# Performance work log

Measured on AMD Instinct MI355X. Metric: run time of the kernel, lower is better.

The kernel has to match this reference:

```python
import jax, jax.numpy as jnp
import numpy as np

DIM = 768
NUM_HEADS = 12
HEAD_DIM = DIM // NUM_HEADS
WS = 14                       # window_size (14, 14)
N_TOK = WS * WS + 1           # 197 (patches + cls)
NUM_REL = (2 * WS - 1) ** 2 + 3  # 732
SCALE = HEAD_DIM ** -0.5


def _build_rel_index():
    # Faithful port of the BEiT relative_position_index construction.
    coords = np.stack(np.meshgrid(np.arange(WS), np.arange(WS), indexing='ij'))  # (2, WS, WS)
    flat = coords.reshape(2, -1)                                   # (2, WS*WS)
    rel = flat[:, :, None] - flat[:, None, :]                      # (2, P, P)
    rel = rel.transpose(1, 2, 0).astype(np.int64)                  # (P, P, 2)
    rel[:, :, 0] += WS - 1
    rel[:, :, 1] += WS - 1
    rel[:, :, 0] *= 2 * WS - 1
    idx = np.zeros((N_TOK, N_TOK), dtype=np.int64)
    idx[1:, 1:] = rel.sum(-1)
    idx[0, :] = NUM_REL - 3
    idx[:, 0] = NUM_REL - 2
    idx[0, 0] = NUM_REL - 1
    return idx


def setup_inputs() -> dict:
    key = jax.random.key(0)
    ks = jax.random.split(key, 7)
    B = 64
    x = jax.random.normal(ks[0], (B, N_TOK, DIM), dtype=jnp.float32)
    qkv_w = jax.random.normal(ks[1], (3 * DIM, DIM), dtype=jnp.float32) * 0.02
    q_bias = jnp.zeros((DIM,), dtype=jnp.float32)
    v_bias = jnp.zeros((DIM,), dtype=jnp.float32)
    rel_table = jax.random.normal(ks[2], (NUM_REL, NUM_HEADS), dtype=jnp.float32) * 0.02
    proj_w = jax.random.normal(ks[3], (DIM, DIM), dtype=jnp.float32) * 0.02
    proj_b = jnp.zeros((DIM,), dtype=jnp.float32)
    rel_index = jnp.asarray(_build_rel_index())  # (N, N) int64
    return {"x": x, "qkv_w": qkv_w, "q_bias": q_bias, "v_bias": v_bias,
            "rel_table": rel_table, "proj_w": proj_w, "proj_b": proj_b,
            "rel_index": rel_index}


def reference(x, qkv_w, q_bias, v_bias, rel_table, proj_w, proj_b, rel_index):
    B, N, C = x.shape
    # qkv bias = concat(q_bias, zeros, v_bias)
    qkv_b = jnp.concatenate([q_bias, jnp.zeros_like(v_bias), v_bias])
    qkv = x @ qkv_w.T + qkv_b                       # (B, N, 3C)
    qkv = qkv.reshape(B, N, 3, NUM_HEADS, HEAD_DIM).transpose(2, 0, 3, 1, 4)
    q, k, v = qkv[0], qkv[1], qkv[2]                # each (B, H, N, hd)
    attn = jnp.einsum('bhqd,bhkd->bhqk', q * SCALE, k)
    # relative position bias gathered from table: (N, N, H) -> (H, N, N)
    bias = rel_table[rel_index].transpose(2, 0, 1)
    attn = attn + bias[None]
    attn = jax.nn.softmax(attn, axis=-1)
    out = jnp.einsum('bhqk,bhkd->bhqd', attn, v)    # (B, H, N, hd)
    out = out.transpose(0, 2, 1, 3).reshape(B, N, -1)
    return out @ proj_w.T + proj_b
```

## Files before the change

### kernel.cpp

```cpp
#include <hip/hip_runtime.h>
#include <stdint.h>

#define NTOK 197
#define HD 64
#define NH 12
#define CDIM 768
#define BB 64
#define MTOT (BB*NTOK)
#define MPAD 12672
#define SCALE 0.125f
#define BTP 208

typedef __attribute__((ext_vector_type(8))) short short8;
typedef __attribute__((ext_vector_type(4))) float f32x4;
typedef unsigned short us;

__device__ __forceinline__ us f2b(float f){
    union { float f; uint32_t u; } v; v.f = f;
    uint32_t u = v.u;
    uint32_t r = u + 0x7fffu + ((u >> 16) & 1u);
    return (us)(r >> 16);
}

__device__ __forceinline__ float b2f(us b){
    union { uint32_t u; float f; } v; v.u = ((uint32_t)b) << 16;
    return v.f;
}

__device__ __forceinline__ void gload16(const us* g, us* l){
    __builtin_amdgcn_global_load_lds((const __attribute__((address_space(1))) void*)g,
                                     (__attribute__((address_space(3))) void*)l, 16, 0, 0);
}

#define LGKM0_BAR() do{ asm volatile("s_waitcnt lgkmcnt(0)" ::: "memory"); \
                        __builtin_amdgcn_s_barrier(); }while(0)

__device__ __forceinline__ void cvt4(const float* in, us* out, int i){
    float4 v = ((const float4*)in)[i];
    ushort4 o;
    o.x = f2b(v.x); o.y = f2b(v.y); o.z = f2b(v.z); o.w = f2b(v.w);
    ((ushort4*)out)[i] = o;
}

__global__ void prep_kernel(const float* __restrict__ x, const float* __restrict__ qkv_w,
                            const float* __restrict__ proj_w,
                            const int* __restrict__ rel_index, const float* __restrict__ rel_table,
                            us* __restrict__ xb, us* __restrict__ wqkv, us* __restrict__ wproj,
                            float* __restrict__ biasT)
{
    const int N1 = MTOT*CDIM/4;
    const int N2 = 3*CDIM*CDIM/4;
    const int N3 = CDIM*CDIM/4;
    const int N4 = BTP*BTP;
    const int total = N1+N2+N3+N4;
    for (int i = blockIdx.x*blockDim.x + threadIdx.x; i < total; i += gridDim.x*blockDim.x){
        if (i < N1) cvt4(x, xb, i);
        else if (i < N1+N2) cvt4(qkv_w, wqkv, i-N1);
        else if (i < N1+N2+N3) cvt4(proj_w, wproj, i-N1-N2);
        else {
            int t = i - N1 - N2 - N3;
            int col = t / BTP, row = t - col*BTP;
            if (row < NTOK && col < NTOK){
                int idx = rel_index[row*NTOK + col];
                #pragma unroll
                for (int h = 0; h < NH; ++h)
                    biasT[((size_t)h*BTP + col)*BTP + row] = rel_table[idx*NH + h];
            } else {
                #pragma unroll
                for (int h = 0; h < NH; ++h)
                    biasT[((size_t)h*BTP + col)*BTP + row] = 0.f;
            }
        }
    }
}

__global__ __launch_bounds__(512,2) void pgemm6_kernel(
    const us* __restrict__ A, const us* __restrict__ Bw,
    us* __restrict__ Qo, us* __restrict__ Ko, us* __restrict__ Vo,
    const float* __restrict__ b0, const float* __restrict__ b2, int ny, int total)
{
    __shared__ __align__(16) us AsB[3][12288];
    us* cbuf = &AsB[2][0];
    const int tid  = threadIdx.x;
    const int lane = tid & 63;
    const int wave = tid >> 6;
    const int wrr = wave >> 2;
    const int wcc = wave & 3;
    const int lr = lane & 15;
    const int g  = lane >> 4;

    const int id  = blockIdx.x;
    const int xcd = id & 7;
    const int jb  = id >> 3;
    const int qs  = total >> 3, rs = total & 7;
    const int Ssp = xcd*qs + (xcd < rs ? xcd : rs);
    const int L   = qs + (xcd < rs ? 1 : 0);
    const int qb  = L >> 6, rb = L & 63;
    const int cnt = qb + (jb < rb ? 1 : 0);
    const int w0  = Ssp + jb*qb + (jb < rb ? jb : rb);
    if (cnt == 0) return;

    int aoff, aldo, bofs[2], bldo[2];
    {
        int c = tid;
        int row = c >> 2, ch = c & 3;
        aoff = row*CDIM + ((ch ^ ((row >> 1) & 3))*8);
        aldo = c*8;
    }
    #pragma unroll
    for (int jj=0;jj<2;jj++){
        int c = tid + jj*512;
        int row = c >> 2, ch = c & 3;
        bofs[jj] = row*CDIM + ((ch ^ ((row >> 1) & 3))*8);
        bldo[jj] = 4096 + c*8;
    }

    const int S = cnt * 24;
    auto stageStep = [&](int x){
        int tt = x / 24, kt = x - tt*24;
        int ww = w0 + tt;
        int bx = ww / ny, by = ww - bx*ny;
        const us* pA = A  + (size_t)(bx*128)*CDIM;
        const us* pB = Bw + (size_t)(by*256)*CDIM;
        int buf = x % 3;
        gload16(pA + aoff + kt*32, &AsB[buf][aldo]);
        #pragma unroll
        for (int jj=0;jj<2;jj++) gload16(pB + bofs[jj] + kt*32, &AsB[buf][bldo[jj]]);
    };

    stageStep(0);
    if (S > 1) stageStep(1);
    int s = 0;

    const int co = 8*(g ^ ((lr >> 1) & 3));

    #pragma unroll 1
    for (int tt = 0; tt < cnt; ++tt){
        const int w  = w0 + tt;
        const int bx = w / ny, by = w - bx*ny;
        const int m0 = bx*128, n0 = by*256;
        const int whc = n0 / CDIM;
        float addf[4];
        const float sclf = (whc == 0) ? SCALE : 1.f;
        #pragma unroll
        for (int nt=0;nt<4;nt++){
            int n = n0 + wcc*64 + nt*16 + lr;
            int hn = n - whc*CDIM;
            addf[nt] = (whc == 0) ? b0[hn] : (whc == 2 ? b2[hn] : 0.f);
        }

        f32x4 acc[4][4];
        #pragma unroll
        for (int i=0;i<4;i++)
            #pragma unroll
            for (int jj=0;jj<4;jj++) acc[i][jj] = (f32x4){0.f,0.f,0.f,0.f};

        #pragma unroll 1
        for (int kt = 0; kt < 24; ++kt){
            if (s == S-1) asm volatile("s_waitcnt vmcnt(0)" ::: "memory");
            else          asm volatile("s_waitcnt vmcnt(3)" ::: "memory");
            __builtin_amdgcn_s_barrier();
            if (s + 2 < S) stageStep(s + 2);
            const us* la = &AsB[s % 3][0];
            const us* lb = &AsB[s % 3][4096];
            short8 af[4], bf[4];
            #pragma unroll
            for (int mt=0;mt<4;mt++)
                af[mt] = *(const short8*)&la[(wrr*64+mt*16+lr)*32 + co];
            #pragma unroll
            for (int nt=0;nt<4;nt++)
                bf[nt] = *(const short8*)&lb[(wcc*64+nt*16+lr)*32 + co];
            __builtin_amdgcn_s_setprio(1);
            #pragma unroll
            for (int mt=0;mt<4;mt++)
                #pragma unroll
                for (int nt=0;nt<4;nt++)
                    acc[mt][nt] = __builtin_amdgcn_mfma_f32_16x16x32_bf16(af[mt], bf[nt], acc[mt][nt], 0,0,0);
            __builtin_amdgcn_s_setprio(0);
            ++s;
        }

        LGKM0_BAR();

        const us* outp = (whc == 0 ? Qo : (whc == 1 ? Ko : Vo));
        #pragma unroll 1
        for (int ph = 0; ph < 4; ++ph){
            const int half  = ph & 1;
            const int rhalf = ph >> 1;
            if (wrr == rhalf && (wcc >> 1) == half){
                #pragma unroll
                for (int mt=0;mt<4;mt++)
                    #pragma unroll
                    for (int rr=0;rr<4;rr++){
                        int row = mt*16 + g*4 + rr;
                        #pragma unroll
                        for (int nt=0;nt<4;nt++){
                            int col = (wcc & 1)*64 + nt*16 + lr;
                            cbuf[row*132 + col] = f2b((acc[mt][nt][rr] + addf[nt]) * sclf);
                        }
                    }
            }
            LGKM0_BAR();
            #pragma unroll
            for (int p=0;p<2;p++){
                int c = tid + p*512;
                int row = c >> 4, ch = c & 15;
                int m = m0 + rhalf*64 + row;
                if (m < MTOT){
                    short8 vv = *(const short8*)&cbuf[row*132 + ch*8];
                    int n = n0 + half*128 + ch*8;
                    int hn = n - whc*CDIM;
                    int h  = hn >> 6, d0 = hn & 63;
                    int bidx = m / NTOK;
                    int tok  = m - bidx*NTOK;
                    size_t off = ((size_t)((bidx*NH + h)*NTOK + tok))*HD + d0;
                    *(short8*)((us*)outp + off) = vv;
                }
            }
            LGKM0_BAR();
        }
    }
}

__global__ __launch_bounds__(256) void proj_gemm_kernel(
    const us* __restrict__ A, const us* __restrict__ Bw,
    float* __restrict__ Cout, const float* __restrict__ b0, int ny)
{
    __shared__ __align__(16) us lds[32768];
    us* As = lds;
    us* Bs = lds + 16384;
    const int tid  = threadIdx.x;
    const int lane = tid & 63;
    const int wave = tid >> 6;
    const int wr = wave >> 1, wc = wave & 1;
    const int lr = lane & 15;
    const int g  = lane >> 4;

    const int NB   = gridDim.x;
    const int base = NB >> 3;
    const int rem  = NB & 7;
    const int id   = blockIdx.x;
    const int xcd  = id & 7;
    const int qq   = id >> 3;
    const int start = (xcd < rem) ? xcd*(base+1) : rem*(base+1) + (xcd-rem)*base;
    const int w    = start + qq;
    const int bx   = w / ny;
    const int by   = w - bx*ny;
    const int m0 = bx * 128;
    const int n0 = by * 128;
    const int NT = CDIM / 128;

    const int row0 = tid >> 4;
    const int cg   = (tid & 15) ^ row0;

    float addf[4];
    #pragma unroll
    for (int nt=0;nt<4;nt++) addf[nt] = b0[n0 + wc*64 + nt*16 + lr];

    f32x4 acc[4][4];
    #pragma unroll
    for (int i=0;i<4;i++)
        #pragma unroll
        for (int j=0;j<4;j++) acc[i][j] = (f32x4){0.f,0.f,0.f,0.f};

    const us* gA = A  + (size_t)(m0 + row0)*CDIM + cg*8;
    const us* gB = Bw + (size_t)(n0 + row0)*CDIM + cg*8;

    #pragma unroll 1
    for (int kt = 0; kt < NT; ++kt){
        __syncthreads();
        #pragma unroll
        for (int j=0;j<8;j++){
            gload16(gA + (size_t)j*16*CDIM + kt*128, As + tid*8 + j*2048);
            gload16(gB + (size_t)j*16*CDIM + kt*128, Bs + tid*8 + j*2048);
        }
        __syncthreads();
        #pragma unroll
        for (int kk=0; kk<4; ++kk){
            const int co = 8*((kk*4 + g) ^ lr);
            short8 af[4], bf[4];
            #pragma unroll
            for (int mt=0;mt<4;mt++)
                af[mt] = *(const short8*)&As[(wr*64+mt*16+lr)*128 + co];
            #pragma unroll
            for (int nt=0;nt<4;nt++)
                bf[nt] = *(const short8*)&Bs[(wc*64+nt*16+lr)*128 + co];
            __builtin_amdgcn_s_setprio(1);
            #pragma unroll
            for (int mt=0;mt<4;mt++)
                #pragma unroll
                for (int nt=0;nt<4;nt++)
                    acc[mt][nt] = __builtin_amdgcn_mfma_f32_16x16x32_bf16(af[mt], bf[nt], acc[mt][nt], 0,0,0);
            __builtin_amdgcn_s_setprio(0);
        }
    }

    __syncthreads();
    #pragma unroll
    for (int mt=0;mt<4;mt++)
        #pragma unroll
        for (int r=0;r<4;r++){
            int row = wr*64 + mt*16 + g*4 + r;
            #pragma unroll
            for (int nt=0;nt<4;nt++){
                int col = wc*64 + nt*16 + lr;
                lds[row*132 + col] = f2b(acc[mt][nt][r] + addf[nt]);
            }
        }
    __syncthreads();
    #pragma unroll
    for (int j=0;j<8;j++){
        int c2  = tid + j*256;
        int row = c2 >> 4;
        int ch  = c2 & 15;
        int m = m0 + row;
        if (m >= MTOT) continue;
        short8 vv = *(const short8*)&lds[row*132 + ch*8];
        int n = n0 + ch*8;
        float4 f0, f1;
        f0.x = b2f((us)vv[0]); f0.y = b2f((us)vv[1]); f0.z = b2f((us)vv[2]); f0.w = b2f((us)vv[3]);
        f1.x = b2f((us)vv[4]); f1.y = b2f((us)vv[5]); f1.z = b2f((us)vv[6]); f1.w = b2f((us)vv[7]);
        *(float4*)&Cout[(size_t)m*CDIM + n]     = f0;
        *(float4*)&Cout[(size_t)m*CDIM + n + 4] = f1;
    }
}

__global__ __launch_bounds__(256) void attn_kernel(
    const us* __restrict__ Q,
    const us* __restrict__ K,
    const us* __restrict__ V,
    const float* __restrict__ biasT,
    us* __restrict__ Ao)
{
    __shared__ us Vt[64][232];
    __shared__ us Ps[4][16][232];
    const int bh = blockIdx.x;
    const int b = bh / NH;
    const int h = bh - b*NH;
    const us* Qh = Q + (size_t)bh*NTOK*HD;
    const us* Kh = K + (size_t)bh*NTOK*HD;
    const us* Vh = V + (size_t)bh*NTOK*HD;
    const float* bT = biasT + (size_t)h*BTP*BTP;
    const int tid = threadIdx.x, lane = tid & 63, wave = tid >> 6;
    const int lr = lane & 15, g = lane >> 4, ko = g*8;

    for (int i = tid; i < 64*232/2; i += 256) ((uint32_t*)Vt)[i] = 0;
    __syncthreads();
    {
        int d0 = (tid & 7) * 8;
        for (int t = tid >> 3; t < NTOK; t += 32){
            short8 v = *(const short8*)&Vh[t*HD + d0];
            #pragma unroll
            for (int j=0;j<8;j++) Vt[d0+j][t] = (us)v[j];
        }
    }
    __syncthreads();

    for (int s = wave; s < 13; s += 4){
        int qrow = s*16 + lr; qrow = qrow > 196 ? 196 : qrow;
        short8 qa0 = *(const short8*)&Qh[qrow*HD + ko];
        short8 qa1 = *(const short8*)&Qh[qrow*HD + 32 + ko];
        f32x4 S[13];
        #pragma unroll
        for (int t=0;t<13;t++){
            int kc = t*16 + lr; kc = kc > 196 ? 196 : kc;
            short8 kb0 = *(const short8*)&Kh[kc*HD + ko];
            short8 kb1 = *(const short8*)&Kh[kc*HD + 32 + ko];
            f32x4 a = (f32x4){0.f,0.f,0.f,0.f};
            a = __builtin_amdgcn_mfma_f32_16x16x32_bf16(qa0, kb0, a, 0,0,0);
            a = __builtin_amdgcn_mfma_f32_16x16x32_bf16(qa1, kb1, a, 0,0,0);
            S[t] = a;
        }
        float rmax[4] = {-3e38f,-3e38f,-3e38f,-3e38f};
        #pragma unroll
        for (int t=0;t<13;t++){
            int col = t*16 + lr;
            bool cok = col < NTOK;
            float4 b4 = *(const float4*)&bT[(size_t)col*BTP + s*16 + g*4];
            #pragma unroll
            for (int r=0;r<4;r++){
                float xv = S[t][r] + ((const float*)&b4)[r];
                xv = cok ? xv : -1e30f;
                S[t][r] = xv;
                rmax[r] = fmaxf(rmax[r], xv);
            }
        }
        #pragma unroll
        for (int r=0;r<4;r++)
            #pragma unroll
            for (int msk=1; msk<16; msk<<=1)
                rmax[r] = fmaxf(rmax[r], __shfl_xor(rmax[r], msk));
        float rsum[4] = {0.f,0.f,0.f,0.f};
        #pragma unroll
        for (int t=0;t<13;t++)
            #pragma unroll
            for (int r=0;r<4;r++){
                float e = __expf(S[t][r] - rmax[r]);
                S[t][r] = e;
                rsum[r] += e;
            }
        #pragma unroll
        for (int r=0;r<4;r++){
            #pragma unroll
            for (int msk=1; msk<16; msk<<=1)
                rsum[r] += __shfl_xor(rsum[r], msk);
            rsum[r] = 1.f / rsum[r];
        }
        #pragma unroll
        for (int t=0;t<13;t++)
            #pragma unroll
            for (int r=0;r<4;r++)
                Ps[wave][g*4+r][t*16+lr] = f2b(S[t][r] * rsum[r]);
        #pragma unroll
        for (int r=0;r<4;r++) Ps[wave][g*4+r][208+lr] = 0;
        asm volatile("s_waitcnt lgkmcnt(0)" ::: "memory");
        f32x4 pv[4];
        #pragma unroll
        for (int nt=0;nt<4;nt++) pv[nt] = (f32x4){0.f,0.f,0.f,0.f};
        #pragma unroll
        for (int ks=0; ks<7; ks++){
            int k0 = ks*32 + ko;
            short8 pa = *(const short8*)&Ps[wave][lr][k0];
            #pragma unroll
            for (int nt=0;nt<4;nt++){
                short8 vb = *(const short8*)&Vt[nt*16+lr][k0];
                pv[nt] = __builtin_amdgcn_mfma_f32_16x16x32_bf16(pa, vb, pv[nt], 0,0,0);
            }
        }
        #pragma unroll
        for (int nt=0;nt<4;nt++)
            #pragma unroll
            for (int r=0;r<4;r++)
                Ps[wave][g*4+r][nt*16+lr] = f2b(pv[nt][r]);
        asm volatile("s_waitcnt lgkmcnt(0)" ::: "memory");
        #pragma unroll
        for (int p=0;p<2;p++){
            int c = lane + p*64;
            int row = c >> 3, ch = c & 7;
            int tok = s*16 + row;
            if (tok < NTOK){
                short8 vv = *(const short8*)&Ps[wave][row][ch*8];
                *(short8*)&Ao[(size_t)(b*NTOK + tok)*CDIM + h*HD + ch*8] = vv;
            }
        }
    }
}

extern "C" void kernel_launch(void* const* d_in, const int* in_sizes, int n_in,
                              void* d_out, int out_size, void* d_ws, size_t ws_size,
                              hipStream_t stream)
{
    const float* x        = (const float*)d_in[0];
    const float* qkv_w    = (const float*)d_in[1];
    const float* q_bias   = (const float*)d_in[2];
    const float* v_bias   = (const float*)d_in[3];
    const float* rel_tab  = (const float*)d_in[4];
    const float* proj_w   = (const float*)d_in[5];
    const float* proj_b   = (const float*)d_in[6];
    const int*   rel_idx  = (const int*)d_in[7];
    float* out = (float*)d_out;

    char* w = (char*)d_ws;
    us* xb    = (us*)w; w += (size_t)MPAD*CDIM*2;
    us* wqkv  = (us*)w; w += (size_t)3*CDIM*CDIM*2;
    us* wproj = (us*)w; w += (size_t)CDIM*CDIM*2;
    us* Qb    = (us*)w; w += (size_t)BB*NH*NTOK*HD*2;
    us* Kb    = (us*)w; w += (size_t)BB*NH*NTOK*HD*2;
    us* Vb    = (us*)w; w += (size_t)BB*NH*NTOK*HD*2;
    float* biasT = (float*)w; w += (size_t)NH*BTP*BTP*4;
    us* aob   = (us*)w; w += (size_t)MPAD*CDIM*2;

    prep_kernel<<<2048, 256, 0, stream>>>(x, qkv_w, proj_w, rel_idx, rel_tab,
                                          xb, wqkv, wproj, biasT);

    pgemm6_kernel<<<512, 512, 0, stream>>>(xb, wqkv, Qb, Kb, Vb, q_bias, v_bias, 9, 891);
    attn_kernel<<<BB*NH, 256, 0, stream>>>(Qb, Kb, Vb, biasT, aob);
    proj_gemm_kernel<<<594, 256, 0, stream>>>(aob, wproj, out, proj_b, 6);
}
```

Before: 152.4 us.

## Load QKV weight fragments directly into registers instead of staging through LDS

The QKV projection GEMM no longer stages the weight (B) tile in shared memory. Each wave now loads its MFMA B fragments straight from global memory into double-buffered registers, while only the A tile still goes through a triple-buffered LDS ring. The LDS footprint drops to a small A ring plus a separate epilogue buffer, and the k-loop is unrolled by two to alternate between the register buffers. The trade-off is that weight reuse across the two row-waves is lost, so each weight element is read from global/L2 twice with uncoalesced 16-byte per-lane loads, and more vector registers are live.

```diff
diff --git a/kernel.cpp b/kernel.cpp
--- a/kernel.cpp
+++ b/kernel.cpp
@@ -74,13 +74,13 @@
     }
 }
 
-__global__ __launch_bounds__(512,2) void pgemm6_kernel(
+__global__ __launch_bounds__(512,2) void pgemm7_kernel(
     const us* __restrict__ A, const us* __restrict__ Bw,
     us* __restrict__ Qo, us* __restrict__ Ko, us* __restrict__ Vo,
     const float* __restrict__ b0, const float* __restrict__ b2, int ny, int total)
 {
-    __shared__ __align__(16) us AsB[3][12288];
-    us* cbuf = &AsB[2][0];
+    __shared__ __align__(16) us AsB[3][4096];
+    __shared__ __align__(16) us cbuf[64*132];
     const int tid  = threadIdx.x;
     const int lane = tid & 63;
     const int wave = tid >> 6;
@@ -100,36 +100,38 @@
     const int w0  = Ssp + jb*qb + (jb < rb ? jb : rb);
     if (cnt == 0) return;
 
-    int aoff, aldo, bofs[2], bldo[2];
+    int aoff, aldo;
     {
         int c = tid;
         int row = c >> 2, ch = c & 3;
         aoff = row*CDIM + ((ch ^ ((row >> 1) & 3))*8);
         aldo = c*8;
     }
+    int colOff[4];
     #pragma unroll
-    for (int jj=0;jj<2;jj++){
-        int c = tid + jj*512;
-        int row = c >> 2, ch = c & 3;
-        bofs[jj] = row*CDIM + ((ch ^ ((row >> 1) & 3))*8);
-        bldo[jj] = 4096 + c*8;
-    }
+    for (int nt=0;nt<4;nt++)
+        colOff[nt] = (wcc*64 + nt*16 + lr)*CDIM + g*8;
 
     const int S = cnt * 24;
-    auto stageStep = [&](int x){
+    auto stageA = [&](int x){
         int tt = x / 24, kt = x - tt*24;
         int ww = w0 + tt;
-        int bx = ww / ny, by = ww - bx*ny;
-        const us* pA = A  + (size_t)(bx*128)*CDIM;
-        const us* pB = Bw + (size_t)(by*256)*CDIM;
-        int buf = x % 3;
-        gload16(pA + aoff + kt*32, &AsB[buf][aldo]);
-        #pragma unroll
-        for (int jj=0;jj<2;jj++) gload16(pB + bofs[jj] + kt*32, &AsB[buf][bldo[jj]]);
+        int bx = ww / ny;
+        const us* pA = A + (size_t)(bx*128)*CDIM;
+        gload16(pA + aoff + kt*32, &AsB[x % 3][aldo]);
     };
 
-    stageStep(0);
-    if (S > 1) stageStep(1);
+    short8 B0[4], B1[4];
+    #define LOADB(DST, X) do{ \
+        int _x=(X); int _tt=_x/24, _kt=_x-_tt*24; \
+        int _ww=w0+_tt; int _bx=_ww/ny; int _by=_ww-_bx*ny; \
+        const us* _pB = Bw + (size_t)(_by*256)*CDIM + _kt*32; \
+        _Pragma("unroll") \
+        for (int nt=0;nt<4;nt++) DST[nt] = *(const short8*)(_pB + colOff[nt]); \
+    }while(0)
+
+    LOADB(B0, 0); stageA(0);
+    LOADB(B1, 1); stageA(1);
     int s = 0;
 
     const int co = 8*(g ^ ((lr >> 1) & 3));
@@ -155,30 +157,32 @@
             #pragma unroll
             for (int jj=0;jj<4;jj++) acc[i][jj] = (f32x4){0.f,0.f,0.f,0.f};
 
+        #define QSTEP(BREG) do{ \
+            if (s == S-1) asm volatile("s_waitcnt vmcnt(0)" ::: "memory"); \
+            else          asm volatile("s_waitcnt vmcnt(5)" ::: "memory"); \
+            __builtin_amdgcn_s_barrier(); \
+            const us* la = &AsB[s % 3][0]; \
+            short8 af[4]; \
+            _Pragma("unroll") \
+            for (int mt=0;mt<4;mt++) \
+                af[mt] = *(const short8*)&la[(wrr*64+mt*16+lr)*32 + co]; \
+            __builtin_amdgcn_s_setprio(1); \
+            _Pragma("unroll") \
+            for (int mt=0;mt<4;mt++) \
+                _Pragma("unroll") \
+                for (int nt=0;nt<4;nt++) \
+                    acc[mt][nt] = __builtin_amdgcn_mfma_f32_16x16x32_bf16(af[mt], BREG[nt], acc[mt][nt], 0,0,0); \
+            __builtin_amdgcn_s_setprio(0); \
+            if (s + 2 < S){ LOADB(BREG, s+2); stageA(s+2); } \
+            ++s; \
+        }while(0)
+
         #pragma unroll 1
-        for (int kt = 0; kt < 24; ++kt){
-            if (s == S-1) asm volatile("s_waitcnt vmcnt(0)" ::: "memory");
-            else          asm volatile("s_waitcnt vmcnt(3)" ::: "memory");
-            __builtin_amdgcn_s_barrier();
-            if (s + 2 < S) stageStep(s + 2);
-            const us* la = &AsB[s % 3][0];
-            const us* lb = &AsB[s % 3][4096];
-            short8 af[4], bf[4];
-            #pragma unroll
-            for (int mt=0;mt<4;mt++)
-                af[mt] = *(const short8*)&la[(wrr*64+mt*16+lr)*32 + co];
-            #pragma unroll
-            for (int nt=0;nt<4;nt++)
-                bf[nt] = *(const short8*)&lb[(wcc*64+nt*16+lr)*32 + co];
-            __builtin_amdgcn_s_setprio(1);
-            #pragma unroll
-            for (int mt=0;mt<4;mt++)
-                #pragma unroll
-                for (int nt=0;nt<4;nt++)
-                    acc[mt][nt] = __builtin_amdgcn_mfma_f32_16x16x32_bf16(af[mt], bf[nt], acc[mt][nt], 0,0,0);
-            __builtin_amdgcn_s_setprio(0);
-            ++s;
-        }
+        for (int it = 0; it < 12; ++it){
+            QSTEP(B0);
+            QSTEP(B1);
+        }
+        #undef QSTEP
 
         LGKM0_BAR();
 
@@ -220,6 +224,7 @@
             LGKM0_BAR();
         }
     }
+    #undef LOADB
 }
 
 __global__ __launch_bounds__(256) void proj_gemm_kernel(
@@ -473,7 +478,7 @@
     prep_kernel<<<2048, 256, 0, stream>>>(x, qkv_w, proj_w, rel_idx, rel_tab,
                                           xb, wqkv, wproj, biasT);
 
-    pgemm6_kernel<<<512, 512, 0, stream>>>(xb, wqkv, Qb, Kb, Vb, q_bias, v_bias, 9, 891);
+    pgemm7_kernel<<<512, 512, 0, stream>>>(xb, wqkv, Qb, Kb, Vb, q_bias, v_bias, 9, 891);
     attn_kernel<<<BB*NH, 256, 0, stream>>>(Qb, Kb, Vb, biasT, aob);
     proj_gemm_kernel<<<594, 256, 0, stream>>>(aob, wproj, out, proj_b, 6);
 }
```

Result: slower. 201.2 us (+32.0%).
